# Optimization experiments

Measured on AMD Instinct MI355X. Metric: run time of the kernel, lower is better.

## Reference

```python
import jax, jax.numpy as jnp
import numpy as np

NUM_MEMORIES = 4096
HIDDEN_DIM = 64
TEMPERATURE = 0.5
SHRINK_THRES = 0.0025
EPS = 1e-12


def _l2_normalize(v, axis=-1):
    # matches torch F.normalize: v / max(||v||_2, eps)
    n = jnp.sqrt(jnp.sum(v * v, axis=axis, keepdims=True))
    return v / jnp.maximum(n, EPS)


def _hard_shrink_relu(w, lambd):
    # relu(w - lambd) * w / (|w - lambd| + eps)
    d = w - lambd
    return jax.nn.relu(d) * w / (jnp.abs(d) + EPS)


def setup_inputs() -> dict:
    key = jax.random.key(0)
    kx, km = jax.random.split(key)
    x = jax.random.normal(kx, (16, 2048, HIDDEN_DIM), dtype=jnp.float32)
    # xavier_uniform for (num_memories, hidden_dim)
    bound = float(np.sqrt(6.0 / (NUM_MEMORIES + HIDDEN_DIM)))
    memories = jax.random.uniform(km, (NUM_MEMORIES, HIDDEN_DIM), dtype=jnp.float32,
                                  minval=-bound, maxval=bound)
    return {"x": x, "memories": memories}


def reference(x, memories):
    # cosine similarity addressing
    x_n = _l2_normalize(x, axis=-1)                      # [B,S,D]
    m_n = _l2_normalize(memories, axis=-1)               # [M,D]
    logits = jnp.einsum('bsd,md->bsm', x_n, m_n)         # [B,S,M]
    weight = jax.nn.softmax(logits / TEMPERATURE, axis=-1)
    # hard-shrink sparsification + L1 renormalization
    weight = _hard_shrink_relu(weight, SHRINK_THRES)
    l1 = jnp.sum(jnp.abs(weight), axis=-1, keepdims=True)
    weight = weight / jnp.maximum(l1, EPS)
    read = jnp.einsum('bsm,md->bsd', weight, memories)   # [B,S,D]
    return read, weight
```

## Files before the change

kernel.cpp:

```cpp
#include <hip/hip_runtime.h>
#include <hip/hip_bf16.h>


#define NM 4096
#define HD 64
#define NROWS 32768

typedef short bf16x8 __attribute__((ext_vector_type(8)));
typedef float f32x4  __attribute__((ext_vector_type(4)));

__global__ __launch_bounds__(256) void prep_rows(const float* __restrict__ src,
                                                 ushort* __restrict__ dst,
                                                 float scale) {
    const int wave = threadIdx.x >> 6, lane = threadIdx.x & 63;
    const long row = (long)blockIdx.x * 4 + wave;
    float v = src[row * HD + lane];
    float s = v * v;
#pragma unroll
    for (int o = 32; o; o >>= 1) s += __shfl_xor(s, o, 64);
    const float inv = scale / fmaxf(sqrtf(s), 1e-12f);
    __hip_bfloat16 h = __float2bfloat16(v * inv);
    dst[row * HD + lane] = *reinterpret_cast<ushort*>(&h);
}

__global__ __launch_bounds__(256) void prep_m_swz(const float* __restrict__ mem,
                                                  ushort* __restrict__ mbs) {
    const int wave = threadIdx.x >> 6, lane = threadIdx.x & 63;
    const int row = blockIdx.x * 4 + wave;
    float v = mem[row * HD + lane];
    float s = v * v;
#pragma unroll
    for (int o = 32; o; o >>= 1) s += __shfl_xor(s, o, 64);
    const float inv = 1.0f / fmaxf(sqrtf(s), 1e-12f);
    __hip_bfloat16 h = __float2bfloat16(v * inv);
    const int t = row >> 4, c = row & 15;
    const int k = lane;
    const int f = k >> 5, q = (k >> 3) & 3, j = k & 7;
    mbs[(long)t * 1024 + f * 512 + (q * 16 + c) * 8 + j] =
        *reinterpret_cast<ushort*>(&h);
}

__global__ __launch_bounds__(512, 4) void k_ps(const ushort* __restrict__ xb,
                                               const ushort* __restrict__ mbs,
                                               const float* __restrict__ mem,
                                               float* __restrict__ out_w,
                                               float* __restrict__ out_read) {
    const int tid = threadIdx.x;
    const int wv = tid >> 6, lane = tid & 63;
    const int m0 = blockIdx.x * 16;

    __shared__ float sS[4][16];
    __shared__ float sL[4][16];
    __shared__ uint  sD[4];
    __shared__ float sred[4][16][64];

    const float4 z4 = make_float4(0.0f, 0.0f, 0.0f, 0.0f);

    if (wv >= 4) {
        const int sw = wv - 4;
        float4* base = (float4*)(out_w + (long)m0 * NM);
#pragma unroll 8
        for (int it = 0; it < 64; it++)
            base[it * 256 + sw * 64 + lane] = z4;
        if (sw == 0) {
            float4* rb = (float4*)(out_read + (long)m0 * HD);
#pragma unroll
            for (int it = 0; it < 4; it++) rb[it * 64 + lane] = z4;
        }
        __syncthreads();
        __syncthreads();
        const uint anyd = sD[0] | sD[1] | sD[2] | sD[3];
        if (anyd) {
            __syncthreads();
            __syncthreads();
        }
        return;
    }

    const int q = lane >> 4, c = lane & 15;
    const int nbase = wv * 1024;
    const bf16x8 a0 = *(const bf16x8*)(xb + (long)(m0 + c) * HD + q * 8);
    const bf16x8 a1 = *(const bf16x8*)(xb + (long)(m0 + c) * HD + q * 8 + 32);
    const ushort* mstrip = mbs + (long)(wv * 64) * 1024;

    float tmax8[8];
    float sm[4] = {0.0f, 0.0f, 0.0f, 0.0f};
    for (int g = 0; g < 8; g++) {
        float tm = -1e30f;
#pragma unroll 4
        for (int ii = 0; ii < 8; ii++) {
            const int i = g * 8 + ii;
            const ushort* mc = mstrip + (long)i * 1024 + lane * 8;
            const bf16x8 b0 = *(const bf16x8*)(mc);
            const bf16x8 b1 = *(const bf16x8*)(mc + 512);
            f32x4 t = {0.0f, 0.0f, 0.0f, 0.0f};
            t = __builtin_amdgcn_mfma_f32_16x16x32_bf16(a0, b0, t, 0, 0, 0);
            t = __builtin_amdgcn_mfma_f32_16x16x32_bf16(a1, b1, t, 0, 0, 0);
            tm = fmaxf(tm, fmaxf(fmaxf(t[0], t[1]), fmaxf(t[2], t[3])));
#pragma unroll
            for (int r = 0; r < 4; r++) sm[r] += __expf(t[r]);
        }
        tmax8[g] = tm;
    }
#pragma unroll
    for (int o = 1; o < 16; o <<= 1)
#pragma unroll
        for (int r = 0; r < 4; r++) sm[r] += __shfl_xor(sm[r], o, 64);
    if (c == 0)
#pragma unroll
        for (int r = 0; r < 4; r++) sS[wv][q * 4 + r] = sm[r];
    __syncthreads();
    float rS[4], tmin = 1e30f;
#pragma unroll
    for (int r = 0; r < 4; r++) {
        const float S = sS[0][q * 4 + r] + sS[1][q * 4 + r] +
                        sS[2][q * 4 + r] + sS[3][q * 4 + r];
        rS[r] = 1.0f / S;
        const float tau = __logf(0.0025f * S) - 1e-3f;
        tmin = fminf(tmin, tau);
    }
    uint dmask = 0;
#pragma unroll
    for (int g = 0; g < 8; g++)
        if (__ballot(tmax8[g] > tmin)) dmask |= 1u << g;
    if (lane == 0) sD[wv] = dmask;
    __syncthreads();
    const uint anyd = sD[0] | sD[1] | sD[2] | sD[3];

    if (!anyd) return;

    float l1[4] = {0.0f, 0.0f, 0.0f, 0.0f};
    for (int g = 0; g < 8; g++) {
        if (!((dmask >> g) & 1u)) continue;
        for (int ii = 0; ii < 8; ii++) {
            const int i = g * 8 + ii;
            const ushort* mc = mstrip + (long)i * 1024 + lane * 8;
            const bf16x8 b0 = *(const bf16x8*)(mc);
            const bf16x8 b1 = *(const bf16x8*)(mc + 512);
            f32x4 t = {0.0f, 0.0f, 0.0f, 0.0f};
            t = __builtin_amdgcn_mfma_f32_16x16x32_bf16(a0, b0, t, 0, 0, 0);
            t = __builtin_amdgcn_mfma_f32_16x16x32_bf16(a1, b1, t, 0, 0, 0);
#pragma unroll
            for (int r = 0; r < 4; r++) {
                float w = __expf(t[r]) * rS[r];
                float d = w - 0.0025f;
                l1[r] += __fdividef(fmaxf(d, 0.0f) * w, fabsf(d) + 1e-12f);
            }
        }
    }
#pragma unroll
    for (int o = 1; o < 16; o <<= 1)
#pragma unroll
        for (int r = 0; r < 4; r++) l1[r] += __shfl_xor(l1[r], o, 64);
    if (c == 0)
#pragma unroll
        for (int r = 0; r < 4; r++) sL[wv][q * 4 + r] = l1[r];
    __syncthreads();
    float rL[4];
#pragma unroll
    for (int r = 0; r < 4; r++)
        rL[r] = 1.0f / fmaxf(sL[0][q * 4 + r] + sL[1][q * 4 + r] +
                             sL[2][q * 4 + r] + sL[3][q * 4 + r], 1e-12f);

    float racc[16];
#pragma unroll
    for (int r = 0; r < 16; r++) racc[r] = 0.0f;
    float* wbase = out_w + (long)(m0 + q * 4) * NM + c;
    for (int i = 0; i < 64; i++) {
        const int n0 = nbase + i * 16;
        const ushort* mc = mstrip + (long)i * 1024 + lane * 8;
        const bf16x8 b0 = *(const bf16x8*)(mc);
        const bf16x8 b1 = *(const bf16x8*)(mc + 512);
        f32x4 t = {0.0f, 0.0f, 0.0f, 0.0f};
        t = __builtin_amdgcn_mfma_f32_16x16x32_bf16(a0, b0, t, 0, 0, 0);
        t = __builtin_amdgcn_mfma_f32_16x16x32_bf16(a1, b1, t, 0, 0, 0);
        float wf[4];
#pragma unroll
        for (int r = 0; r < 4; r++) {
            float w  = __expf(t[r]) * rS[r];
            float d  = w - 0.0025f;
            float sh = __fdividef(fmaxf(d, 0.0f) * w, fabsf(d) + 1e-12f);
            wf[r] = sh * rL[r];
            wbase[(long)r * NM + n0] = wf[r];
        }
        const bool nz = (wf[0] != 0.0f) | (wf[1] != 0.0f) |
                        (wf[2] != 0.0f) | (wf[3] != 0.0f);
        unsigned long long mask = __ballot(nz);
        while (mask) {
            const int j = __ffsll((long long)mask) - 1;
            mask &= (mask - 1);
            const int qj = j >> 4, cj = j & 15;
            float b0v = __shfl(wf[0], j, 64), b1v = __shfl(wf[1], j, 64);
            float b2v = __shfl(wf[2], j, 64), b3v = __shfl(wf[3], j, 64);
            const float mv = mem[(long)(n0 + cj) * HD + lane];
            switch (qj) {
                case 0: racc[0]  += b0v * mv; racc[1]  += b1v * mv;
                        racc[2]  += b2v * mv; racc[3]  += b3v * mv; break;
                case 1: racc[4]  += b0v * mv; racc[5]  += b1v * mv;
                        racc[6]  += b2v * mv; racc[7]  += b3v * mv; break;
                case 2: racc[8]  += b0v * mv; racc[9]  += b1v * mv;
                        racc[10] += b2v * mv; racc[11] += b3v * mv; break;
                default: racc[12] += b0v * mv; racc[13] += b1v * mv;
                         racc[14] += b2v * mv; racc[15] += b3v * mv; break;
            }
        }
    }

#pragma unroll
    for (int r = 0; r < 16; r++) sred[wv][r][lane] = racc[r];
    __syncthreads();
#pragma unroll
    for (int rr = 0; rr < 4; rr++) {
        const int row = wv * 4 + rr;
        const float v = sred[0][row][lane] + sred[1][row][lane] +
                        sred[2][row][lane] + sred[3][row][lane];
        out_read[(long)(m0 + row) * HD + lane] = v;
    }
}

extern "C" void kernel_launch(void* const* d_in, const int* in_sizes, int n_in,
                              void* d_out, int out_size, void* d_ws, size_t ws_size,
                              hipStream_t stream) {
    const float* x   = (const float*)d_in[0];
    const float* mem = (const float*)d_in[1];
    ushort* xb       = (ushort*)d_ws;
    ushort* mbs      = xb + (long)NROWS * HD;
    float* out_read  = (float*)d_out;
    float* out_w     = out_read + (long)NROWS * HD;

    prep_rows<<<NROWS / 4, 256, 0, stream>>>(x, xb, 2.0f);
    prep_m_swz<<<NM / 4, 256, 0, stream>>>(mem, mbs);
    k_ps<<<NROWS / 16, 512, 0, stream>>>(xb, mbs, mem, out_w, out_read);
}
```

Before: 537.0 us.

## Certify all-zero shrunk weights with a Jensen bound to skip the similarity GEMM

Precomputes the sum of the normalized memory rows and, for each row block, tests a Jensen lower bound on the softmax denominator using the dot of x with that sum. The bound is sound because every cosine is at most 1. When the bound shows every weight falls below the shrink threshold, the block only writes zeros and skips both MFMA passes and the exps. Blocks that fail the test fall back to the full computation, which no longer uses per-group skip masks. The kernel also shrinks to 256 threads, with all waves sharing the zero-fill, and adds an atomic reduction into a workspace vector.

```diff
diff --git a/kernel.cpp b/kernel.cpp
--- a/kernel.cpp
+++ b/kernel.cpp
@@ -11,7 +11,9 @@
 
 __global__ __launch_bounds__(256) void prep_rows(const float* __restrict__ src,
                                                  ushort* __restrict__ dst,
-                                                 float scale) {
+                                                 float scale,
+                                                 float* __restrict__ Mv) {
+    if (blockIdx.x == 0 && threadIdx.x < 64) Mv[threadIdx.x] = 0.0f;
     const int wave = threadIdx.x >> 6, lane = threadIdx.x & 63;
     const long row = (long)blockIdx.x * 4 + wave;
     float v = src[row * HD + lane];
@@ -24,7 +26,9 @@
 }
 
 __global__ __launch_bounds__(256) void prep_m_swz(const float* __restrict__ mem,
-                                                  ushort* __restrict__ mbs) {
+                                                  ushort* __restrict__ mbs,
+                                                  float* __restrict__ Mv) {
+    __shared__ float sM[4][64];
     const int wave = threadIdx.x >> 6, lane = threadIdx.x & 63;
     const int row = blockIdx.x * 4 + wave;
     float v = mem[row * HD + lane];
@@ -32,50 +36,63 @@
 #pragma unroll
     for (int o = 32; o; o >>= 1) s += __shfl_xor(s, o, 64);
     const float inv = 1.0f / fmaxf(sqrtf(s), 1e-12f);
-    __hip_bfloat16 h = __float2bfloat16(v * inv);
+    const float nv = v * inv;
+    __hip_bfloat16 h = __float2bfloat16(nv);
     const int t = row >> 4, c = row & 15;
     const int k = lane;
     const int f = k >> 5, q = (k >> 3) & 3, j = k & 7;
     mbs[(long)t * 1024 + f * 512 + (q * 16 + c) * 8 + j] =
         *reinterpret_cast<ushort*>(&h);
-}
-
-__global__ __launch_bounds__(512, 4) void k_ps(const ushort* __restrict__ xb,
-                                               const ushort* __restrict__ mbs,
-                                               const float* __restrict__ mem,
-                                               float* __restrict__ out_w,
-                                               float* __restrict__ out_read) {
+    sM[wave][lane] = nv;
+    __syncthreads();
+    if (wave == 0)
+        atomicAdd(&Mv[lane],
+                  sM[0][lane] + sM[1][lane] + sM[2][lane] + sM[3][lane]);
+}
+
+__global__ __launch_bounds__(256, 4) void k_zero(const float* __restrict__ x,
+                                                 const float* __restrict__ Mv,
+                                                 const ushort* __restrict__ xb,
+                                                 const ushort* __restrict__ mbs,
+                                                 const float* __restrict__ mem,
+                                                 float* __restrict__ out_w,
+                                                 float* __restrict__ out_read) {
     const int tid = threadIdx.x;
     const int wv = tid >> 6, lane = tid & 63;
     const int m0 = blockIdx.x * 16;
 
     __shared__ float sS[4][16];
     __shared__ float sL[4][16];
-    __shared__ uint  sD[4];
+    __shared__ int   sFail[4];
     __shared__ float sred[4][16][64];
 
+    {
+        const int r16 = lane >> 4;
+        const int k16 = lane & 15;
+        const long row = (long)m0 + wv * 4 + r16;
+        const float4 xv = *(const float4*)(x + row * HD + k16 * 4);
+        const float4 mv = *(const float4*)(Mv + k16 * 4);
+        float dot = xv.x * mv.x + xv.y * mv.y + xv.z * mv.z + xv.w * mv.w;
+        float nn  = xv.x * xv.x + xv.y * xv.y + xv.z * xv.z + xv.w * xv.w;
+#pragma unroll
+        for (int o = 1; o < 16; o <<= 1) {
+            dot += __shfl_xor(dot, o, 64);
+            nn  += __shfl_xor(nn,  o, 64);
+        }
+        const bool pass = dot >= -573.44f * fmaxf(sqrtf(nn), 1e-12f);
+        const unsigned long long bal = __ballot(!pass);
+        if (lane == 0) sFail[wv] = (bal != 0ull);
+    }
+
     const float4 z4 = make_float4(0.0f, 0.0f, 0.0f, 0.0f);
-
-    if (wv >= 4) {
-        const int sw = wv - 4;
-        float4* base = (float4*)(out_w + (long)m0 * NM);
+    float4* base = (float4*)(out_w + (long)m0 * NM);
 #pragma unroll 8
-        for (int it = 0; it < 64; it++)
-            base[it * 256 + sw * 64 + lane] = z4;
-        if (sw == 0) {
-            float4* rb = (float4*)(out_read + (long)m0 * HD);
-#pragma unroll
-            for (int it = 0; it < 4; it++) rb[it * 64 + lane] = z4;
-        }
-        __syncthreads();
-        __syncthreads();
-        const uint anyd = sD[0] | sD[1] | sD[2] | sD[3];
-        if (anyd) {
-            __syncthreads();
-            __syncthreads();
-        }
-        return;
-    }
+    for (int it = 0; it < 64; it++)
+        base[it * 256 + tid] = z4;
+    ((float4*)(out_read + (long)m0 * HD))[tid] = z4;
+
+    __syncthreads();
+    if (!(sFail[0] | sFail[1] | sFail[2] | sFail[3])) return;
 
     const int q = lane >> 4, c = lane & 15;
     const int nbase = wv * 1024;
@@ -83,24 +100,16 @@
     const bf16x8 a1 = *(const bf16x8*)(xb + (long)(m0 + c) * HD + q * 8 + 32);
     const ushort* mstrip = mbs + (long)(wv * 64) * 1024;
 
-    float tmax8[8];
     float sm[4] = {0.0f, 0.0f, 0.0f, 0.0f};
-    for (int g = 0; g < 8; g++) {
-        float tm = -1e30f;
-#pragma unroll 4
-        for (int ii = 0; ii < 8; ii++) {
-            const int i = g * 8 + ii;
-            const ushort* mc = mstrip + (long)i * 1024 + lane * 8;
-            const bf16x8 b0 = *(const bf16x8*)(mc);
-            const bf16x8 b1 = *(const bf16x8*)(mc + 512);
-            f32x4 t = {0.0f, 0.0f, 0.0f, 0.0f};
-            t = __builtin_amdgcn_mfma_f32_16x16x32_bf16(a0, b0, t, 0, 0, 0);
-            t = __builtin_amdgcn_mfma_f32_16x16x32_bf16(a1, b1, t, 0, 0, 0);
-            tm = fmaxf(tm, fmaxf(fmaxf(t[0], t[1]), fmaxf(t[2], t[3])));
-#pragma unroll
-            for (int r = 0; r < 4; r++) sm[r] += __expf(t[r]);
-        }
-        tmax8[g] = tm;
+    for (int i = 0; i < 64; i++) {
+        const ushort* mc = mstrip + (long)i * 1024 + lane * 8;
+        const bf16x8 b0 = *(const bf16x8*)(mc);
+        const bf16x8 b1 = *(const bf16x8*)(mc + 512);
+        f32x4 t = {0.0f, 0.0f, 0.0f, 0.0f};
+        t = __builtin_amdgcn_mfma_f32_16x16x32_bf16(a0, b0, t, 0, 0, 0);
+        t = __builtin_amdgcn_mfma_f32_16x16x32_bf16(a1, b1, t, 0, 0, 0);
+#pragma unroll
+        for (int r = 0; r < 4; r++) sm[r] += __expf(t[r]);
     }
 #pragma unroll
     for (int o = 1; o < 16; o <<= 1)
@@ -110,42 +119,25 @@
 #pragma unroll
         for (int r = 0; r < 4; r++) sS[wv][q * 4 + r] = sm[r];
     __syncthreads();
-    float rS[4], tmin = 1e30f;
-#pragma unroll
-    for (int r = 0; r < 4; r++) {
-        const float S = sS[0][q * 4 + r] + sS[1][q * 4 + r] +
-                        sS[2][q * 4 + r] + sS[3][q * 4 + r];
-        rS[r] = 1.0f / S;
-        const float tau = __logf(0.0025f * S) - 1e-3f;
-        tmin = fminf(tmin, tau);
-    }
-    uint dmask = 0;
-#pragma unroll
-    for (int g = 0; g < 8; g++)
-        if (__ballot(tmax8[g] > tmin)) dmask |= 1u << g;
-    if (lane == 0) sD[wv] = dmask;
-    __syncthreads();
-    const uint anyd = sD[0] | sD[1] | sD[2] | sD[3];
-
-    if (!anyd) return;
+    float rS[4];
+#pragma unroll
+    for (int r = 0; r < 4; r++)
+        rS[r] = 1.0f / (sS[0][q * 4 + r] + sS[1][q * 4 + r] +
+                        sS[2][q * 4 + r] + sS[3][q * 4 + r]);
 
     float l1[4] = {0.0f, 0.0f, 0.0f, 0.0f};
-    for (int g = 0; g < 8; g++) {
-        if (!((dmask >> g) & 1u)) continue;
-        for (int ii = 0; ii < 8; ii++) {
-            const int i = g * 8 + ii;
-            const ushort* mc = mstrip + (long)i * 1024 + lane * 8;
-            const bf16x8 b0 = *(const bf16x8*)(mc);
-            const bf16x8 b1 = *(const bf16x8*)(mc + 512);
-            f32x4 t = {0.0f, 0.0f, 0.0f, 0.0f};
-            t = __builtin_amdgcn_mfma_f32_16x16x32_bf16(a0, b0, t, 0, 0, 0);
-            t = __builtin_amdgcn_mfma_f32_16x16x32_bf16(a1, b1, t, 0, 0, 0);
-#pragma unroll
-            for (int r = 0; r < 4; r++) {
-                float w = __expf(t[r]) * rS[r];
-                float d = w - 0.0025f;
-                l1[r] += __fdividef(fmaxf(d, 0.0f) * w, fabsf(d) + 1e-12f);
-            }
+    for (int i = 0; i < 64; i++) {
+        const ushort* mc = mstrip + (long)i * 1024 + lane * 8;
+        const bf16x8 b0 = *(const bf16x8*)(mc);
+        const bf16x8 b1 = *(const bf16x8*)(mc + 512);
+        f32x4 t = {0.0f, 0.0f, 0.0f, 0.0f};
+        t = __builtin_amdgcn_mfma_f32_16x16x32_bf16(a0, b0, t, 0, 0, 0);
+        t = __builtin_amdgcn_mfma_f32_16x16x32_bf16(a1, b1, t, 0, 0, 0);
+#pragma unroll
+        for (int r = 0; r < 4; r++) {
+            float w = __expf(t[r]) * rS[r];
+            float d = w - 0.0025f;
+            l1[r] += __fdividef(fmaxf(d, 0.0f) * w, fabsf(d) + 1e-12f);
         }
     }
 #pragma unroll
@@ -225,10 +217,11 @@
     const float* mem = (const float*)d_in[1];
     ushort* xb       = (ushort*)d_ws;
     ushort* mbs      = xb + (long)NROWS * HD;
+    float*  Mv       = (float*)(mbs + (long)NM * HD);
     float* out_read  = (float*)d_out;
     float* out_w     = out_read + (long)NROWS * HD;
 
-    prep_rows<<<NROWS / 4, 256, 0, stream>>>(x, xb, 2.0f);
-    prep_m_swz<<<NM / 4, 256, 0, stream>>>(mem, mbs);
-    k_ps<<<NROWS / 16, 512, 0, stream>>>(xb, mbs, mem, out_w, out_read);
-}
+    prep_rows<<<NROWS / 4, 256, 0, stream>>>(x, xb, 2.0f, Mv);
+    prep_m_swz<<<NM / 4, 256, 0, stream>>>(mem, mbs, Mv);
+    k_zero<<<NROWS / 16, 256, 0, stream>>>(x, Mv, xb, mbs, mem, out_w, out_read);
+}
```

New measurement: 563.2 us. +4.9%, slower.
